# Performance work log

Hardware: AMD Instinct MI355X
Metric: run time of the kernel (lower is better)

Reference implementation:

```python
import jax, jax.numpy as jnp
import numpy as np

T = S = 1024
B = 8
HID = 1024
H = 16
D = HID // H          # head_size = 64
RELK = 16             # max relative position (clip window)
NEG = -1e9


def setup_inputs() -> dict:
    key = jax.random.key(0)
    ks = jax.random.split(key, 12)
    inv = 1.0 / np.sqrt(HID)
    inp = {
        'q': jax.random.normal(ks[0], (T, B, HID), jnp.float32),
        'k': jax.random.normal(ks[1], (S, B, HID), jnp.float32),
        'v': jax.random.normal(ks[2], (S, B, HID), jnp.float32),
        # additive float mask (B,T,S): causal, masked positions = -1e9
        'mask': jnp.broadcast_to(jnp.triu(jnp.full((T, S), NEG, jnp.float32), k=1), (B, T, S)),
        'Wq': jax.random.normal(ks[3], (HID, HID), jnp.float32) * inv,
        'bq': jnp.zeros((HID,), jnp.float32),
        'Wk': jax.random.normal(ks[4], (HID, HID), jnp.float32) * inv,
        'bk': jnp.zeros((HID,), jnp.float32),
        'Wv': jax.random.normal(ks[5], (HID, HID), jnp.float32) * inv,
        'bv': jnp.zeros((HID,), jnp.float32),
        'Wo': jax.random.normal(ks[6], (HID, HID), jnp.float32) * inv,
        'bo': jnp.zeros((HID,), jnp.float32),
        'rel_k_table': jax.random.normal(ks[7], (2 * RELK + 1, D), jnp.float32) * 0.02,
        'rel_v_table': jax.random.normal(ks[8], (2 * RELK + 1, D), jnp.float32) * 0.02,
    }
    return inp


def _rel_index(t, s):
    # clipped relative position index (t, s) -> [0, 2*RELK]
    return jnp.clip(jnp.arange(s)[None, :] - jnp.arange(t)[:, None], -RELK, RELK) + RELK


def reference(q, k, v, mask, Wq, bq, Wk, bk, Wv, bv, Wo, bo, rel_k_table, rel_v_table):
    t, b, _ = q.shape
    scaling = D ** -0.5
    # projections; torch Linear: x @ W^T + b, here weights stored (in,out)
    qh = ((q @ Wq + bq) * scaling).reshape(t, b * H, D).transpose(1, 0, 2)  # (BH,T,D)
    kh = (k @ Wk + bk).reshape(-1, b * H, D).transpose(1, 0, 2)            # (BH,S,D)
    vh = (v @ Wv + bv).reshape(-1, b * H, D).transpose(1, 0, 2)            # (BH,S,D)
    s = kh.shape[1]

    score = jnp.einsum('ntd,nsd->nts', qh, kh)                 # (BH,T,S)
    idx = _rel_index(t, s)
    rel_k = rel_k_table[idx]                                   # (T,S,D)
    score = score + jnp.einsum('ntd,tsd->nts', qh, rel_k)      # relative-pos bias on scores

    score = (score.reshape(b, H, t, s) + mask[:, None]).reshape(b * H, t, s)
    attn = jax.nn.softmax(score, axis=-1)                      # dropout=0 (eval)

    o = jnp.einsum('nts,nsd->ntd', attn, vh)                   # (BH,T,D)
    rel_v = rel_v_table[idx]                                   # (T,S,D)
    o = o + jnp.einsum('nts,tsd->ntd', attn, rel_v)            # relative-pos bias on values

    o = o.transpose(1, 0, 2).reshape(t, b, H * D)              # (T,B,hidden)
    return o @ Wo + bo
```

## Files before the change

kernel.cpp:

```cpp
#include <hip/hip_runtime.h>

typedef unsigned short u16;
typedef __bf16 bf16x8 __attribute__((ext_vector_type(8)));
typedef __bf16 bf16x4v __attribute__((ext_vector_type(4)));
typedef short s16x4 __attribute__((ext_vector_type(4)));
typedef unsigned short u16x8 __attribute__((ext_vector_type(8)));
typedef unsigned short u16x4 __attribute__((ext_vector_type(4)));
typedef float f32x4 __attribute__((ext_vector_type(4)));


__device__ __forceinline__ u16 f2bf(float f) {
  union { float f; unsigned u; } v; v.f = f;
  unsigned r = v.u + 0x7fffu + ((v.u >> 16) & 1u);
  return (u16)(r >> 16);
}
__device__ __forceinline__ u16x8 pack_trunc8(float4 a, float4 b) {
  u16x8 t;
  t[0] = (u16)(__float_as_uint(a.x) >> 16); t[1] = (u16)(__float_as_uint(a.y) >> 16);
  t[2] = (u16)(__float_as_uint(a.z) >> 16); t[3] = (u16)(__float_as_uint(a.w) >> 16);
  t[4] = (u16)(__float_as_uint(b.x) >> 16); t[5] = (u16)(__float_as_uint(b.y) >> 16);
  t[6] = (u16)(__float_as_uint(b.z) >> 16); t[7] = (u16)(__float_as_uint(b.w) >> 16);
  return t;
}
__device__ __forceinline__ void barrier_lgkm() {
  __asm__ volatile("s_waitcnt lgkmcnt(0)\ns_barrier" ::: "memory");
}
typedef const __attribute__((address_space(1))) void* gas_ptr;
typedef __attribute__((address_space(3))) void* las_ptr;
__device__ __forceinline__ void load_lds16(const void* g, void* l) {
  __builtin_amdgcn_global_load_lds((gas_ptr)g, (las_ptr)l, 16, 0, 0);
}
__device__ __forceinline__ f32x4 mfma16(u16x4 a, u16x4 b, f32x4 c) {
#if __has_builtin(__builtin_amdgcn_mfma_f32_16x16x16_bf16)
  return __builtin_amdgcn_mfma_f32_16x16x16_bf16(
      __builtin_bit_cast(bf16x4v, a), __builtin_bit_cast(bf16x4v, b), c, 0, 0, 0);
#elif __has_builtin(__builtin_amdgcn_mfma_f32_16x16x16bf16_1k)
  return __builtin_amdgcn_mfma_f32_16x16x16bf16_1k(
      __builtin_bit_cast(s16x4, a), __builtin_bit_cast(s16x4, b), c, 0, 0, 0);
#else
  f32x4 d;
  __asm__ volatile("v_mfma_f32_16x16x16_bf16 %0, %1, %2, %3"
                   : "=v"(d) : "v"(a), "v"(b), "v"(c));
  return d;
#endif
}

__device__ __forceinline__ void transpose_body(const float* in, u16* out) {
  __shared__ u16 tile[64][65];
  const int r0 = blockIdx.y * 64, c0 = blockIdx.x * 64;
  const int tid = threadIdx.x;
  const int tr = tid >> 4, tc4 = (tid & 15) * 4;
#pragma unroll
  for (int p = 0; p < 4; ++p) {
    int r = tr + p * 16;
    float4 vv = *(const float4*)&in[(size_t)(r0 + r) * 1024 + c0 + tc4];
    tile[r][tc4 + 0] = f2bf(vv.x); tile[r][tc4 + 1] = f2bf(vv.y);
    tile[r][tc4 + 2] = f2bf(vv.z); tile[r][tc4 + 3] = f2bf(vv.w);
  }
  __syncthreads();
#pragma unroll
  for (int p = 0; p < 4; ++p) {
    int rr = tr + p * 16;
    ushort4 ov;
    ov.x = tile[tc4 + 0][rr]; ov.y = tile[tc4 + 1][rr];
    ov.z = tile[tc4 + 2][rr]; ov.w = tile[tc4 + 3][rr];
    *(ushort4*)&out[(size_t)(c0 + rr) * 1024 + r0 + tc4] = ov;
  }
}
__global__ __launch_bounds__(256) void transpose_cvt3_kernel(
    const float* w0, const float* w1, const float* w2,
    u16* o0, u16* o1, u16* o2)
{
  const float* in = blockIdx.z == 0 ? w0 : (blockIdx.z == 1 ? w1 : w2);
  u16* out = blockIdx.z == 0 ? o0 : (blockIdx.z == 1 ? o1 : o2);
  transpose_body(in, out);
}
__global__ __launch_bounds__(256) void transpose_cvt_kernel(
    const float* in, u16* out) { transpose_body(in, out); }

__global__ __launch_bounds__(256) void cvt2_kernel(
    const float* __restrict__ a, const float* __restrict__ b,
    u16* __restrict__ oa, u16* __restrict__ ob)
{
  const float* in = blockIdx.z ? b : a;
  u16* out = blockIdx.z ? ob : oa;
  const int n8 = (8192 * 1024) / 8;
  for (int i = blockIdx.x * 256 + threadIdx.x; i < n8; i += gridDim.x * 256) {
    float4 x = ((const float4*)in)[i * 2];
    float4 y = ((const float4*)in)[i * 2 + 1];
    *(u16x8*)&out[(size_t)i * 8] = pack_trunc8(x, y);
  }
}

struct GemmArgs {
  const u16* A; const u16* BT; const float* bias; void* out;
  float scale; int mode;
};

__global__ __launch_bounds__(256) void gemm_lds_kernel(GemmArgs g0, GemmArgs g1)
{
  __shared__ __align__(16) u16 smem[128 * 136];
  const GemmArgs g = blockIdx.z ? g1 : g0;
  const u16* __restrict__ A = g.A;
  const u16* __restrict__ BT = g.BT;
  const int tid = threadIdx.x;
  const int wave = tid >> 6, lane = tid & 63;
  const int quad = lane >> 4, l16 = lane & 15;
  const int wave_m = wave >> 1, wave_n = wave & 1;
  const int m0 = blockIdx.x * 128, n0 = blockIdx.y * 128;

  const int crow = tid >> 2;
  const int cq = (((tid & 3) ^ ((tid >> 3) & 3))) * 8;
  const int qswr = (quad ^ ((l16 >> 1) & 3)) * 8;

  f32x4 acc[4][4] = {};

  auto STAGE = [&](int bo, int kb) {
    const size_t ka = (size_t)kb * 32 + cq;
    load_lds16(&A [(size_t)(m0 + crow)      * 1024 + ka], &smem[bo + tid * 8]);
    load_lds16(&A [(size_t)(m0 + 64 + crow) * 1024 + ka], &smem[bo + 2048 + tid * 8]);
    load_lds16(&BT[(size_t)(n0 + crow)      * 1024 + ka], &smem[bo + 4096 + tid * 8]);
    load_lds16(&BT[(size_t)(n0 + 64 + crow) * 1024 + ka], &smem[bo + 6144 + tid * 8]);
  };

  STAGE(0, 0);
  __syncthreads();
  int cur = 0;
  for (int kb = 0; kb < 32; ++kb) {
    if (kb + 1 < 32) STAGE(cur ^ 8192, kb + 1);
    const u16* As = &smem[cur];
    const u16* Bs = &smem[cur + 4096];
    bf16x8 af[4], bfr[4];
#pragma unroll
    for (int mt = 0; mt < 4; ++mt)
      af[mt] = *(const bf16x8*)&As[(wave_m * 64 + mt * 16 + l16) * 32 + qswr];
#pragma unroll
    for (int nt = 0; nt < 4; ++nt)
      bfr[nt] = *(const bf16x8*)&Bs[(wave_n * 64 + nt * 16 + l16) * 32 + qswr];
#pragma unroll
    for (int mt = 0; mt < 4; ++mt)
#pragma unroll
      for (int nt = 0; nt < 4; ++nt)
        acc[mt][nt] = __builtin_amdgcn_mfma_f32_16x16x32_bf16(af[mt], bfr[nt], acc[mt][nt], 0, 0, 0);
    __syncthreads();
    cur ^= 8192;
  }

  const float scale = g.scale;
  if (g.mode == 0) {
#pragma unroll
    for (int mt = 0; mt < 4; ++mt)
#pragma unroll
      for (int nt = 0; nt < 4; ++nt) {
        int nn = n0 + wave_n * 64 + nt * 16 + l16;
        float bval = g.bias[nn];
#pragma unroll
        for (int reg = 0; reg < 4; ++reg) {
          int mm = m0 + wave_m * 64 + mt * 16 + quad * 4 + reg;
          ((float*)g.out)[(size_t)mm * 1024 + nn] = (acc[mt][nt][reg] + bval) * scale;
        }
      }
  } else {
    __syncthreads();
    u16* Cs = smem;
#pragma unroll
    for (int mt = 0; mt < 4; ++mt)
#pragma unroll
      for (int nt = 0; nt < 4; ++nt) {
        int nnl = wave_n * 64 + nt * 16 + l16;
        float bval = g.bias[n0 + nnl];
#pragma unroll
        for (int reg = 0; reg < 4; ++reg) {
          int mml = wave_m * 64 + mt * 16 + quad * 4 + reg;
          Cs[mml * 136 + nnl] = f2bf((acc[mt][nt][reg] + bval) * scale);
        }
      }
    __syncthreads();
    u16* out = (u16*)g.out;
    if (g.mode == 1) {
      int row = tid >> 1, half = tid & 1;
      int mm = m0 + row;
      int tt = mm >> 3, bbv = mm & 7;
      int hh = (n0 >> 6) + half;
      u16* dst = &out[(((size_t)(bbv * 16 + hh)) * 1024 + tt) * 64];
#pragma unroll
      for (int i = 0; i < 8; ++i)
        *(u16x8*)&dst[i * 8] = *(const u16x8*)&Cs[row * 136 + half * 64 + i * 8];
    } else {
      int t0 = m0 >> 3;
#pragma unroll
      for (int rr = 0; rr < 4; ++rr) {
        int rid = tid * 4 + rr;
        int nnv = rid >> 3, bbv = rid & 7;
        int hh = (n0 + nnv) >> 6, dd = (n0 + nnv) & 63;
        u16* dst = &out[(((size_t)(bbv * 16 + hh)) * 64 + dd) * 1024 + t0];
        u16x8 w0, w1;
#pragma unroll
        for (int t = 0; t < 8; ++t) w0[t] = Cs[(t * 8 + bbv) * 136 + nnv];
#pragma unroll
        for (int t = 0; t < 8; ++t) w1[t] = Cs[((t + 8) * 8 + bbv) * 136 + nnv];
        *(u16x8*)&dst[0] = w0;
        *(u16x8*)&dst[8] = w1;
      }
    }
  }
}

__global__ __launch_bounds__(256, 4) void attn_kernel(
    const u16* __restrict__ qh, const u16* __restrict__ kh,
    const u16* __restrict__ vt, const float* __restrict__ relk,
    const float* __restrict__ relv, u16* __restrict__ octx)
{
  const int n = blockIdx.x;
  const int q0 = (15 - blockIdx.y) * 64;
  const int tid = threadIdx.x;
  const int wave = tid >> 6, lane = tid & 63;
  const int quad = lane >> 4, l16 = lane & 15;
  const int rowi = wave * 16 + l16;
  const int trow = q0 + rowi;

  __shared__ __align__(16) u16 Ks[64 * 72];
  __shared__ __align__(16) u16 Vs[64 * 72];
  __shared__ float qrelS[64 * 17];
  __shared__ float wvS[17 * 64];
  __shared__ float relvS[17 * 64];

  const int diag = q0 >> 6;
  const int ntiles = diag + 1;

  bf16x8 qf[2];
#pragma unroll
  for (int kc = 0; kc < 2; ++kc)
    qf[kc] = *(const bf16x8*)&qh[((size_t)n * 1024 + trow) * 64 + kc * 32 + quad * 8];

  u16x8 kreg[2], vreg[2];
#pragma unroll
  for (int j = 0; j < 2; ++j) {
    int c = j * 256 + tid;
    kreg[j] = *(const u16x8*)&kh[((size_t)n * 1024 + (c >> 3)) * 64 + (c & 7) * 8];
    vreg[j] = *(const u16x8*)&vt[((size_t)n * 64 + (c >> 3)) * 1024 + (c & 7) * 8];
  }
  for (int i = tid; i < 17 * 64; i += 256) { wvS[i] = relk[i]; relvS[i] = relv[i]; }
  __syncthreads();

  float qreg[16];
#pragma unroll
  for (int kc = 0; kc < 2; ++kc)
#pragma unroll
    for (int jj = 0; jj < 8; ++jj)
      qreg[kc * 8 + jj] = (float)qf[kc][jj];
  float qrel0 = 0.f;
  for (int r = 0; r <= 16; ++r) {
    float s = 0.f;
#pragma unroll
    for (int kc = 0; kc < 2; ++kc)
#pragma unroll
      for (int jj = 0; jj < 8; ++jj)
        s += qreg[kc * 8 + jj] * wvS[r * 64 + kc * 32 + quad * 8 + jj];
    s += __shfl_xor(s, 16);
    s += __shfl_xor(s, 32);
    if (r == 0) qrel0 = s;
    if (quad == 0) qrelS[rowi * 17 + r] = s;
  }
  __syncthreads();
  for (int i = tid; i < 17 * 64; i += 256) wvS[i] = 0.f;
  __syncthreads();

  f32x4 oacc[4] = {};
  float lrow = 0.f;

  for (int st = 0; st < ntiles; ++st) {
    const int s0 = st * 64;
    if (st) barrier_lgkm();
#pragma unroll
    for (int j = 0; j < 2; ++j) {
      int c = j * 256 + tid;
      *(u16x8*)&Ks[(c >> 3) * 72 + (c & 7) * 8] = kreg[j];
      *(u16x8*)&Vs[(c >> 3) * 72 + (c & 7) * 8] = vreg[j];
    }
    barrier_lgkm();
    if (st + 1 < ntiles) {
      int s1 = s0 + 64;
#pragma unroll
      for (int j = 0; j < 2; ++j) {
        int c = j * 256 + tid;
        kreg[j] = *(const u16x8*)&kh[((size_t)n * 1024 + s1 + (c >> 3)) * 64 + (c & 7) * 8];
        vreg[j] = *(const u16x8*)&vt[((size_t)n * 64 + (c >> 3)) * 1024 + s1 + (c & 7) * 8];
      }
    }

    f32x4 sc[4];
#pragma unroll
    for (int j = 0; j < 4; ++j) {
      f32x4 c4 = {};
#pragma unroll
      for (int kc = 0; kc < 2; ++kc) {
        bf16x8 kf = *(const bf16x8*)&Ks[(j * 16 + l16) * 72 + kc * 32 + quad * 8];
        c4 = __builtin_amdgcn_mfma_f32_16x16x32_bf16(kf, qf[kc], c4, 0, 0, 0);
      }
      sc[j] = c4;
    }

    u16x4 pfrag[4];
    if (st < diag - 1) {
#pragma unroll
      for (int j = 0; j < 4; ++j) {
        u16x4 pk;
#pragma unroll
        for (int reg = 0; reg < 4; ++reg) {
          float pv = __expf(sc[j][reg] + qrel0 - 8.f);
          lrow += pv;
          pk[reg] = f2bf(pv);
        }
        pfrag[j] = pk;
      }
    } else {
#pragma unroll
      for (int j = 0; j < 4; ++j) {
        u16x4 pk;
#pragma unroll
        for (int reg = 0; reg < 4; ++reg) {
          int sel = s0 + j * 16 + quad * 4 + reg;
          int dt = trow - sel;
          float pv = 0.f;
          if (dt >= 0) {
            int r = (dt < 16) ? (16 - dt) : 0;
            pv = __expf(sc[j][reg] + qrelS[rowi * 17 + r] - 8.f);
            if (dt < 16) wvS[rowi * 17 + (16 - dt)] = pv;
          }
          lrow += pv;
          pk[reg] = f2bf(pv);
        }
        pfrag[j] = pk;
      }
    }

#pragma unroll
    for (int nt = 0; nt < 4; ++nt)
#pragma unroll
      for (int j = 0; j < 4; ++j) {
        u16x4 vfrag = *(const u16x4*)&Vs[(nt * 16 + l16) * 72 + j * 16 + quad * 4];
        oacc[nt] = mfma16(vfrag, pfrag[j], oacc[nt]);
      }
  }

  lrow += __shfl_xor(lrow, 16);
  lrow += __shfl_xor(lrow, 32);

  float wvr[17];
  float bsum = 0.f;
#pragma unroll
  for (int r = 1; r <= 16; ++r) { wvr[r] = wvS[rowi * 17 + r]; bsum += wvr[r]; }
  wvr[0] = lrow - bsum;
  float linv = 1.f / lrow;

  const int hh = n & 15, bb = n >> 4;
  size_t base = ((size_t)trow * 8 + bb) * 1024 + hh * 64;
#pragma unroll
  for (int nt = 0; nt < 4; ++nt) {
    u16x4 ov;
#pragma unroll
    for (int reg = 0; reg < 4; ++reg) {
      int d = nt * 16 + quad * 4 + reg;
      float rv = 0.f;
#pragma unroll
      for (int r = 0; r <= 16; ++r) rv += wvr[r] * relvS[r * 64 + d];
      ov[reg] = f2bf((oacc[nt][reg] + rv) * linv);
    }
    *(u16x4*)&octx[base + nt * 16 + quad * 4] = ov;
  }
}

extern "C" void kernel_launch(void* const* d_in, const int* in_sizes, int n_in,
                              void* d_out, int out_size, void* d_ws, size_t ws_size,
                              hipStream_t stream) {
  (void)in_sizes; (void)n_in; (void)out_size; (void)ws_size;
  const float* q    = (const float*)d_in[0];
  const float* k    = (const float*)d_in[1];
  const float* v    = (const float*)d_in[2];
  const float* Wq   = (const float*)d_in[4];
  const float* bq   = (const float*)d_in[5];
  const float* Wk   = (const float*)d_in[6];
  const float* bk   = (const float*)d_in[7];
  const float* Wv   = (const float*)d_in[8];
  const float* bv   = (const float*)d_in[9];
  const float* Wo   = (const float*)d_in[10];
  const float* bo   = (const float*)d_in[11];
  const float* relk = (const float*)d_in[12];
  const float* relv = (const float*)d_in[13];
  float* out = (float*)d_out;

  char* ws = (char*)d_ws;
  u16* vt   = (u16*)(ws);
  u16* qh   = (u16*)(ws + ((size_t)16 << 20));
  u16* kh   = (u16*)(ws + ((size_t)32 << 20));
  u16* octx = (u16*)(ws + ((size_t)48 << 20));
  u16* wqt  = (u16*)(ws + ((size_t)48 << 20));
  u16* wkt  = (u16*)(ws + ((size_t)50 << 20));
  u16* wvt  = (u16*)(ws + ((size_t)52 << 20));
  u16* wot  = kh;
  u16* qbf  = (u16*)d_out;
  u16* kbf  = (u16*)d_out + ((size_t)8 << 20);
  u16* vbf  = (u16*)d_out;

  dim3 blk(256);
  transpose_cvt3_kernel<<<dim3(16, 16, 3), blk, 0, stream>>>(Wq, Wk, Wv, wqt, wkt, wvt);

  cvt2_kernel<<<dim3(2048, 1, 2), blk, 0, stream>>>(q, k, qbf, kbf);
  GemmArgs gq{qbf, wqt, bq, qh, 0.125f, 1};
  GemmArgs gk{kbf, wkt, bk, kh, 1.0f,   1};
  gemm_lds_kernel<<<dim3(64, 8, 2), blk, 0, stream>>>(gq, gk);

  cvt2_kernel<<<dim3(2048, 1, 1), blk, 0, stream>>>(v, v, vbf, vbf);
  GemmArgs gv{vbf, wvt, bv, vt, 1.0f, 2};
  gemm_lds_kernel<<<dim3(64, 8, 1), blk, 0, stream>>>(gv, gv);

  attn_kernel<<<dim3(128, 16), blk, 0, stream>>>(qh, kh, vt, relk, relv, octx);

  transpose_cvt_kernel<<<dim3(16, 16), blk, 0, stream>>>(Wo, wot);

  GemmArgs go{octx, wot, bo, out, 1.0f, 0};
  gemm_lds_kernel<<<dim3(64, 8, 1), blk, 0, stream>>>(go, go);
}
```

Baseline: 358.9 us.

## Double-buffer K/V tiles in attention, merge conversions, use exp2 softmax

The attention kernel now keeps two register sets of K/V tiles and prefetches two tiles ahead, so global loads overlap compute across more iterations. The exponential uses exp2f with LOG2E folded into the precomputed relative-position bias and offset, and f2bf uses the hardware bf16 conversion. On the host side, the q/k/v fp32-to-bf16 conversions are merged into one launch by placing vbf in the kh workspace, and the V projection now runs before Q/K. The extra prefetch registers may lower occupancy at launch bound 4.

```diff
diff --git a/kernel.cpp b/kernel.cpp
--- a/kernel.cpp
+++ b/kernel.cpp
@@ -10,9 +10,7 @@
 
 
 __device__ __forceinline__ u16 f2bf(float f) {
-  union { float f; unsigned u; } v; v.f = f;
-  unsigned r = v.u + 0x7fffu + ((v.u >> 16) & 1u);
-  return (u16)(r >> 16);
+  return __builtin_bit_cast(u16, (__bf16)f);
 }
 __device__ __forceinline__ u16x8 pack_trunc8(float4 a, float4 b) {
   u16x8 t;
@@ -78,12 +76,13 @@
 __global__ __launch_bounds__(256) void transpose_cvt_kernel(
     const float* in, u16* out) { transpose_body(in, out); }
 
-__global__ __launch_bounds__(256) void cvt2_kernel(
+__global__ __launch_bounds__(256) void cvt3_kernel(
     const float* __restrict__ a, const float* __restrict__ b,
-    u16* __restrict__ oa, u16* __restrict__ ob)
+    const float* __restrict__ c,
+    u16* __restrict__ oa, u16* __restrict__ ob, u16* __restrict__ oc)
 {
-  const float* in = blockIdx.z ? b : a;
-  u16* out = blockIdx.z ? ob : oa;
+  const float* in = blockIdx.z == 0 ? a : (blockIdx.z == 1 ? b : c);
+  u16* out = blockIdx.z == 0 ? oa : (blockIdx.z == 1 ? ob : oc);
   const int n8 = (8192 * 1024) / 8;
   for (int i = blockIdx.x * 256 + threadIdx.x; i < n8; i += gridDim.x * 256) {
     float4 x = ((const float4*)in)[i * 2];
@@ -218,6 +217,7 @@
   const int quad = lane >> 4, l16 = lane & 15;
   const int rowi = wave * 16 + l16;
   const int trow = q0 + rowi;
+  const float LOG2E = 1.442695040888963f;
 
   __shared__ __align__(16) u16 Ks[64 * 72];
   __shared__ __align__(16) u16 Vs[64 * 72];
@@ -233,13 +233,21 @@
   for (int kc = 0; kc < 2; ++kc)
     qf[kc] = *(const bf16x8*)&qh[((size_t)n * 1024 + trow) * 64 + kc * 32 + quad * 8];
 
-  u16x8 kreg[2], vreg[2];
-#pragma unroll
-  for (int j = 0; j < 2; ++j) {
-    int c = j * 256 + tid;
-    kreg[j] = *(const u16x8*)&kh[((size_t)n * 1024 + (c >> 3)) * 64 + (c & 7) * 8];
-    vreg[j] = *(const u16x8*)&vt[((size_t)n * 64 + (c >> 3)) * 1024 + (c & 7) * 8];
-  }
+  const u16* __restrict__ khn = kh + (size_t)n * 1024 * 64;
+  const u16* __restrict__ vtn = vt + (size_t)n * 64 * 1024;
+
+  u16x8 kA[2], vA[2], kB[2], vB[2];
+  auto LOADT = [&](int s0, u16x8 (&kr)[2], u16x8 (&vr)[2]) {
+#pragma unroll
+    for (int j = 0; j < 2; ++j) {
+      int c = j * 256 + tid;
+      kr[j] = *(const u16x8*)&khn[(size_t)(s0 + (c >> 3)) * 64 + (c & 7) * 8];
+      vr[j] = *(const u16x8*)&vtn[(size_t)(c >> 3) * 1024 + s0 + (c & 7) * 8];
+    }
+  };
+  LOADT(0, kA, vA);
+  if (1 < ntiles) LOADT(64, kB, vB);
+
   for (int i = tid; i < 17 * 64; i += 256) { wvS[i] = relk[i]; relvS[i] = relv[i]; }
   __syncthreads();
 
@@ -259,8 +267,9 @@
         s += qreg[kc * 8 + jj] * wvS[r * 64 + kc * 32 + quad * 8 + jj];
     s += __shfl_xor(s, 16);
     s += __shfl_xor(s, 32);
-    if (r == 0) qrel0 = s;
-    if (quad == 0) qrelS[rowi * 17 + r] = s;
+    float sv = (s - 8.f) * LOG2E;
+    if (r == 0) qrel0 = sv;
+    if (quad == 0) qrelS[rowi * 17 + r] = sv;
   }
   __syncthreads();
   for (int i = tid; i < 17 * 64; i += 256) wvS[i] = 0.f;
@@ -269,26 +278,17 @@
   f32x4 oacc[4] = {};
   float lrow = 0.f;
 
-  for (int st = 0; st < ntiles; ++st) {
-    const int s0 = st * 64;
-    if (st) barrier_lgkm();
+  auto WRITET = [&](u16x8 (&kr)[2], u16x8 (&vr)[2]) {
 #pragma unroll
     for (int j = 0; j < 2; ++j) {
       int c = j * 256 + tid;
-      *(u16x8*)&Ks[(c >> 3) * 72 + (c & 7) * 8] = kreg[j];
-      *(u16x8*)&Vs[(c >> 3) * 72 + (c & 7) * 8] = vreg[j];
-    }
-    barrier_lgkm();
-    if (st + 1 < ntiles) {
-      int s1 = s0 + 64;
-#pragma unroll
-      for (int j = 0; j < 2; ++j) {
-        int c = j * 256 + tid;
-        kreg[j] = *(const u16x8*)&kh[((size_t)n * 1024 + s1 + (c >> 3)) * 64 + (c & 7) * 8];
-        vreg[j] = *(const u16x8*)&vt[((size_t)n * 64 + (c >> 3)) * 1024 + s1 + (c & 7) * 8];
-      }
-    }
-
+      *(u16x8*)&Ks[(c >> 3) * 72 + (c & 7) * 8] = kr[j];
+      *(u16x8*)&Vs[(c >> 3) * 72 + (c & 7) * 8] = vr[j];
+    }
+  };
+
+  auto COMPUTE = [&](int st) {
+    const int s0 = st * 64;
     f32x4 sc[4];
 #pragma unroll
     for (int j = 0; j < 4; ++j) {
@@ -308,7 +308,7 @@
         u16x4 pk;
 #pragma unroll
         for (int reg = 0; reg < 4; ++reg) {
-          float pv = __expf(sc[j][reg] + qrel0 - 8.f);
+          float pv = exp2f(fmaf(sc[j][reg], LOG2E, qrel0));
           lrow += pv;
           pk[reg] = f2bf(pv);
         }
@@ -325,7 +325,7 @@
           float pv = 0.f;
           if (dt >= 0) {
             int r = (dt < 16) ? (16 - dt) : 0;
-            pv = __expf(sc[j][reg] + qrelS[rowi * 17 + r] - 8.f);
+            pv = exp2f(fmaf(sc[j][reg], LOG2E, qrelS[rowi * 17 + r]));
             if (dt < 16) wvS[rowi * 17 + (16 - dt)] = pv;
           }
           lrow += pv;
@@ -342,6 +342,20 @@
         u16x4 vfrag = *(const u16x4*)&Vs[(nt * 16 + l16) * 72 + j * 16 + quad * 4];
         oacc[nt] = mfma16(vfrag, pfrag[j], oacc[nt]);
       }
+  };
+
+  for (int st = 0; st < ntiles; st += 2) {
+    if (st) barrier_lgkm();
+    WRITET(kA, vA);
+    barrier_lgkm();
+    if (st + 2 < ntiles) LOADT((st + 2) * 64, kA, vA);
+    COMPUTE(st);
+    if (st + 1 >= ntiles) break;
+    barrier_lgkm();
+    WRITET(kB, vB);
+    barrier_lgkm();
+    if (st + 3 < ntiles) LOADT((st + 3) * 64, kB, vB);
+    COMPUTE(st + 1);
   }
 
   lrow += __shfl_xor(lrow, 16);
@@ -394,6 +408,7 @@
   u16* vt   = (u16*)(ws);
   u16* qh   = (u16*)(ws + ((size_t)16 << 20));
   u16* kh   = (u16*)(ws + ((size_t)32 << 20));
+  u16* vbf  = kh;
   u16* octx = (u16*)(ws + ((size_t)48 << 20));
   u16* wqt  = (u16*)(ws + ((size_t)48 << 20));
   u16* wkt  = (u16*)(ws + ((size_t)50 << 20));
@@ -401,20 +416,19 @@
   u16* wot  = kh;
   u16* qbf  = (u16*)d_out;
   u16* kbf  = (u16*)d_out + ((size_t)8 << 20);
-  u16* vbf  = (u16*)d_out;
 
   dim3 blk(256);
   transpose_cvt3_kernel<<<dim3(16, 16, 3), blk, 0, stream>>>(Wq, Wk, Wv, wqt, wkt, wvt);
 
-  cvt2_kernel<<<dim3(2048, 1, 2), blk, 0, stream>>>(q, k, qbf, kbf);
+  cvt3_kernel<<<dim3(2048, 1, 3), blk, 0, stream>>>(q, k, v, qbf, kbf, vbf);
+
+  GemmArgs gv{vbf, wvt, bv, vt, 1.0f, 2};
+  gemm_lds_kernel<<<dim3(64, 8, 1), blk, 0, stream>>>(gv, gv);
+
   GemmArgs gq{qbf, wqt, bq, qh, 0.125f, 1};
   GemmArgs gk{kbf, wkt, bk, kh, 1.0f,   1};
   gemm_lds_kernel<<<dim3(64, 8, 2), blk, 0, stream>>>(gq, gk);
 
-  cvt2_kernel<<<dim3(2048, 1, 1), blk, 0, stream>>>(v, v, vbf, vbf);
-  GemmArgs gv{vbf, wvt, bv, vt, 1.0f, 2};
-  gemm_lds_kernel<<<dim3(64, 8, 1), blk, 0, stream>>>(gv, gv);
-
   attn_kernel<<<dim3(128, 16), blk, 0, stream>>>(qh, kh, vt, relk, relv, octx);
 
   transpose_cvt_kernel<<<dim3(16, 16), blk, 0, stream>>>(Wo, wot);
```

After: 360.5 us. About the same (+0.5%).
